# Kernel tuning notes

Hardware: AMD Instinct MI355X
Metric: run time of the kernel (lower is better)

## Reference

```python
import jax, jax.numpy as jnp
import numpy as np

N = 100000          # num nodes
E = 3200000         # num edges (avg degree 32)
G = 64              # num graphs in batch
F_IN = 2            # num_node_features
H = 16              # hidden_size
NUM_LAYERS = 2


def sage_conv(x, src, dst, W_l, b_l, W_r):
    # PyG SAGEConv (mean aggr): out = lin_l(mean_{j in N(i)} x_j) + lin_r(x_i)
    msg = x[src]                                                  # [E, F] gather
    agg = jax.ops.segment_sum(msg, dst, num_segments=N)          # [N, F] scatter-add
    deg = jax.ops.segment_sum(jnp.ones((src.shape[0],), x.dtype), dst, num_segments=N)
    mean = agg / jnp.maximum(deg, 1.0)[:, None]
    return mean @ W_l + b_l + x @ W_r


def setup_inputs() -> dict:
    key = jax.random.key(0)
    ks = jax.random.split(key, 10)
    x = jax.random.normal(ks[0], (N, F_IN), dtype=jnp.float32)
    edge_index = jax.random.randint(ks[1], (2, E), 0, N, dtype=jnp.int64)
    batch = jnp.sort(jax.random.randint(ks[2], (N,), 0, G, dtype=jnp.int64))
    s1 = 1.0 / np.sqrt(F_IN)
    s2 = 1.0 / np.sqrt(H)
    return {
        "x": x,
        "edge_index": edge_index,
        "batch": batch,
        "W1_l": jax.random.uniform(ks[3], (F_IN, H), jnp.float32, -s1, s1),
        "b1_l": jnp.zeros((H,), jnp.float32),
        "W1_r": jax.random.uniform(ks[4], (F_IN, H), jnp.float32, -s1, s1),
        "W2_l": jax.random.uniform(ks[5], (H, H), jnp.float32, -s2, s2),
        "b2_l": jnp.zeros((H,), jnp.float32),
        "W2_r": jax.random.uniform(ks[6], (H, H), jnp.float32, -s2, s2),
        "W_end": jax.random.uniform(ks[7], (H, 1), jnp.float32, -s2, s2),
        "b_end": jnp.zeros((1,), jnp.float32),
    }


def reference(x, edge_index, batch, W1_l, b1_l, W1_r, W2_l, b2_l, W2_r, W_end, b_end):
    src, dst = edge_index[0], edge_index[1]
    h = sage_conv(x, src, dst, W1_l, b1_l, W1_r)                 # conv1
    for _ in range(NUM_LAYERS - 1):
        h = jax.nn.relu(h)
        h = sage_conv(h, src, dst, W2_l, b2_l, W2_r)             # conv2
    h = jax.nn.relu(h)
    # dropout is identity in eval mode
    h = h @ W_end + b_end                                         # [N, 1]
    # global mean pool over graphs
    summed = jax.ops.segment_sum(h, batch, num_segments=G)       # [G, 1]
    counts = jax.ops.segment_sum(jnp.ones((N,), h.dtype), batch, num_segments=G)
    pooled = summed / jnp.maximum(counts, 1.0)[:, None]
    return jax.nn.sigmoid(pooled)                                 # [G, 1]
```

## Files before the change

### kernel.cpp

```cpp
#include <hip/hip_runtime.h>
#include <math.h>

#define NN 100000
#define NE 3200000
#define NG 64
#define HID 16
#define EPB 8192
#define NBLKE ((NE + EPB - 1) / EPB)
#define NBUCK ((NN + 255) / 256)
#define LMAX 10240

typedef unsigned int uint;
typedef float vf2 __attribute__((ext_vector_type(2)));


template <bool HI>
__device__ inline vf2 dec2fp8(uint u) {
#if __has_builtin(__builtin_amdgcn_cvt_pk_f32_fp8)
    return __builtin_amdgcn_cvt_pk_f32_fp8((int)u, HI);
#else
    vf2 r;
    uint b0 = (u >> (HI ? 16 : 0)) & 0xff;
    uint b1 = (u >> (HI ? 24 : 8)) & 0xff;
    uint em0 = b0 & 0x7f, em1 = b1 & 0x7f;
    float v0 = (em0 >= 8) ? __uint_as_float(((em0 >> 3) + 120) << 23 | (em0 & 7) << 20)
                          : (float)em0 * 0.001953125f;
    float v1 = (em1 >= 8) ? __uint_as_float(((em1 >> 3) + 120) << 23 | (em1 & 7) << 20)
                          : (float)em1 * 0.001953125f;
    r.x = (b0 & 0x80) ? -v0 : v0;
    r.y = (b1 & 0x80) ? -v1 : v1;
    return r;
#endif
}

__device__ inline uint enc1fp8(float f) {
    if (!(f > 0.f)) return 0u;
    f = fminf(f, 448.f);
    uint b = __float_as_uint(f);
    int e = (int)(b >> 23) - 127;
    if (e >= -6) {
        uint m = b & 0x7fffffu;
        uint r = (m + 0x7ffffu + ((m >> 20) & 1u)) >> 20;
        uint code = ((uint)(e + 7) << 3) + r;
        return code > 126u ? 126u : code;
    }
    float t = f * 512.f;
    return (uint)(t + 0.5f);
}

template <bool HI>
__device__ inline uint packfp8x2(float a, float b, uint old) {
#if __has_builtin(__builtin_amdgcn_cvt_pk_fp8_f32)
    return (uint)__builtin_amdgcn_cvt_pk_fp8_f32(a, b, (int)old, HI);
#else
    uint v = enc1fp8(a) | (enc1fp8(b) << 8);
    return HI ? ((old & 0x0000ffffu) | (v << 16)) : ((old & 0xffff0000u) | v);
#endif
}

__global__ __launch_bounds__(512) void k_bhist(const int* __restrict__ dst,
                                               int* __restrict__ blockCnt) {
    __shared__ int h[NBUCK];
    int t = threadIdx.x;
    for (int i = t; i < NBUCK; i += 512) h[i] = 0;
    __syncthreads();
    int base = blockIdx.x * EPB;
    int n4 = (min(base + EPB, NE) - base) >> 2;
    const int4* d4 = (const int4*)(dst + base);
    for (int i = t; i < n4; i += 512) {
        int4 v = d4[i];
        atomicAdd(&h[v.x >> 8], 1);
        atomicAdd(&h[v.y >> 8], 1);
        atomicAdd(&h[v.z >> 8], 1);
        atomicAdd(&h[v.w >> 8], 1);
    }
    __syncthreads();
    for (int i = t; i < NBUCK; i += 512)
        blockCnt[i * NBLKE + blockIdx.x] = h[i];
}

__global__ __launch_bounds__(512) void k_bucketscan(int* __restrict__ blockCnt,
                                                    int* __restrict__ bucketTot) {
    __shared__ int a[512];
    int t = threadIdx.x, b = blockIdx.x;
    a[t] = (t < NBLKE) ? blockCnt[b * NBLKE + t] : 0;
    __syncthreads();
    for (int off = 1; off < 512; off <<= 1) {
        int x = a[t] + ((t >= off) ? a[t - off] : 0);
        __syncthreads();
        a[t] = x;
        __syncthreads();
    }
    if (t < NBLKE) blockCnt[b * NBLKE + t] = (t ? a[t - 1] : 0);
    if (t == 0) bucketTot[b] = a[511];
}

__global__ __launch_bounds__(512) void k_basescan(const int* __restrict__ bucketTot,
                                                  int* __restrict__ bucketBase,
                                                  int* __restrict__ offs,
                                                  float* __restrict__ gsum,
                                                  float* __restrict__ gcnt) {
    __shared__ int a[512];
    int t = threadIdx.x;
    if (t < NG) { gsum[t] = 0.f; gcnt[t] = 0.f; }
    a[t] = (t < NBUCK) ? bucketTot[t] : 0;
    __syncthreads();
    for (int off = 1; off < 512; off <<= 1) {
        int x = a[t] + ((t >= off) ? a[t - off] : 0);
        __syncthreads();
        a[t] = x;
        __syncthreads();
    }
    if (t < NBUCK) bucketBase[t] = (t ? a[t - 1] : 0);
    if (t == 0) { bucketBase[NBUCK] = a[511]; offs[NN] = a[511]; }
}

__global__ __launch_bounds__(512) void k_bscatter(const int* __restrict__ src,
                                                  const int* __restrict__ dst,
                                                  const int* __restrict__ blockCnt,
                                                  const int* __restrict__ bucketBase,
                                                  int* __restrict__ pairs) {
    __shared__ int cur[NBUCK];
    int t = threadIdx.x;
    for (int i = t; i < NBUCK; i += 512)
        cur[i] = blockCnt[i * NBLKE + blockIdx.x] + bucketBase[i];
    __syncthreads();
    int base = blockIdx.x * EPB;
    int n4 = (min(base + EPB, NE) - base) >> 2;
    const int4* d4 = (const int4*)(dst + base);
    const int4* s4 = (const int4*)(src + base);
    for (int i = t; i < n4; i += 512) {
        int4 dv = d4[i];
        int4 sv = s4[i];
        int p0 = atomicAdd(&cur[dv.x >> 8], 1);
        pairs[p0] = (sv.x << 8) | (dv.x & 255);
        int p1 = atomicAdd(&cur[dv.y >> 8], 1);
        pairs[p1] = (sv.y << 8) | (dv.y & 255);
        int p2 = atomicAdd(&cur[dv.z >> 8], 1);
        pairs[p2] = (sv.z << 8) | (dv.z & 255);
        int p3 = atomicAdd(&cur[dv.w >> 8], 1);
        pairs[p3] = (sv.w << 8) | (dv.w & 255);
    }
}

__global__ __launch_bounds__(512) void k_fill2c1(
    const int* __restrict__ bucketBase, const int* __restrict__ pairs,
    const float* __restrict__ x,
    const float* __restrict__ W1l, const float* __restrict__ b1l,
    const float* __restrict__ W1r,
    int* __restrict__ offs, int* __restrict__ csr, uint* __restrict__ h8) {
    __shared__ int a[256];
    __shared__ int lcur[256];
    __shared__ int lss[LMAX];
    int t = threadIdx.x, b = blockIdx.x;
    int pb = bucketBase[b], pe = bucketBase[b + 1];
    if (t < 256) a[t] = 0;
    __syncthreads();
    for (int e = pb + t; e < pe; e += 512)
        atomicAdd(&a[pairs[e] & 255], 1);
    __syncthreads();
    for (int off = 1; off < 256; off <<= 1) {
        int v = 0;
        if (t < 256) v = a[t] + ((t >= off) ? a[t - off] : 0);
        __syncthreads();
        if (t < 256) a[t] = v;
        __syncthreads();
    }
    if (t < 256) lcur[t] = t ? a[t - 1] : 0;
    __syncthreads();
    for (int e = pb + t; e < pe; e += 512) {
        int v = pairs[e];
        int s = v >> 8, dl = v & 255;
        int lpos = atomicAdd(&lcur[dl], 1);
        csr[pb + lpos] = s;
        if (lpos < LMAX) lss[lpos] = s;
    }
    __syncthreads();
    if (t < 256) {
        int node = b * 256 + t;
        if (node < NN) {
            int excl = t ? a[t - 1] : 0;
            int cntn = a[t] - excl;
            offs[node] = pb + excl;
            float s0 = 0.f, s1 = 0.f;
            for (int k = 0; k < cntn; ++k) {
                int idx = excl + k;
                int s = (idx < LMAX) ? lss[idx] : csr[pb + idx];
                float2 xv = *(const float2*)(x + 2 * s);
                s0 += xv.x; s1 += xv.y;
            }
            float inv = 1.0f / fmaxf((float)cntn, 1.0f);
            float m0 = s0 * inv, m1 = s1 * inv;
            float x0 = x[2 * node], x1 = x[2 * node + 1];
            float o[16];
#pragma unroll
            for (int h = 0; h < 16; ++h)
                o[h] = fmaxf(m0 * W1l[h] + m1 * W1l[16 + h] + b1l[h]
                           + x0 * W1r[h] + x1 * W1r[16 + h], 0.f);
            uint4 w;
            w.x = packfp8x2<false>(o[0],  o[1],  0u);
            w.x = packfp8x2<true >(o[2],  o[3],  w.x);
            w.y = packfp8x2<false>(o[4],  o[5],  0u);
            w.y = packfp8x2<true >(o[6],  o[7],  w.y);
            w.z = packfp8x2<false>(o[8],  o[9],  0u);
            w.z = packfp8x2<true >(o[10], o[11], w.z);
            w.w = packfp8x2<false>(o[12], o[13], 0u);
            w.w = packfp8x2<true >(o[14], o[15], w.w);
            *(uint4*)(h8 + (size_t)node * 4) = w;
        }
    }
}

__global__ __launch_bounds__(256) void k_conv2pool(
    const int* __restrict__ offs, const int* __restrict__ csr,
    const uint* __restrict__ h8,
    const float* __restrict__ W2l, const float* __restrict__ b2l,
    const float* __restrict__ W2r, const float* __restrict__ Wend,
    const float* __restrict__ bend, const int* __restrict__ batch,
    float* __restrict__ gsum, float* __restrict__ gcnt) {
    __shared__ float sWl[256], sWr[256], sB[HID], sWe[HID];
    __shared__ float sm[64][17], shr[64][17];
    __shared__ float ls[NG], lc[NG];
    int t = threadIdx.x;
    sWl[t] = W2l[t];
    sWr[t] = W2r[t];
    if (t < HID) { sB[t] = b2l[t]; sWe[t] = Wend[t]; }
    if (t < NG) { ls[t] = 0.f; lc[t] = 0.f; }

    int g = t >> 2;
    int l4 = t & 3;
    int gbase = (t & 63) & 60;
    int i = blockIdx.x * 64 + g;
    int beg = 0, end = 0;
    if (i < NN) { beg = offs[i]; end = offs[i + 1]; }
    float a0 = 0.f, a1 = 0.f, a2 = 0.f, a3 = 0.f;
    int kb = beg;
    uint ub[8];
    for (; kb + 8 <= end; kb += 8) {
        int sv0 = csr[kb + l4];
        int sv1 = csr[kb + 4 + l4];
#pragma unroll
        for (int j = 0; j < 4; ++j) {
            int s = __shfl(sv0, gbase + j, 64);
            ub[j] = h8[(size_t)s * 4 + l4];
        }
#pragma unroll
        for (int j = 0; j < 4; ++j) {
            int s = __shfl(sv1, gbase + j, 64);
            ub[4 + j] = h8[(size_t)s * 4 + l4];
        }
#pragma unroll
        for (int j = 0; j < 8; ++j) {
            vf2 p0 = dec2fp8<false>(ub[j]);
            vf2 p1 = dec2fp8<true >(ub[j]);
            a0 += p0.x; a1 += p0.y; a2 += p1.x; a3 += p1.y;
        }
    }
    for (; kb + 4 <= end; kb += 4) {
        int sv = csr[kb + l4];
#pragma unroll
        for (int j = 0; j < 4; ++j) {
            int s = __shfl(sv, gbase + j, 64);
            ub[j] = h8[(size_t)s * 4 + l4];
        }
#pragma unroll
        for (int j = 0; j < 4; ++j) {
            vf2 p0 = dec2fp8<false>(ub[j]);
            vf2 p1 = dec2fp8<true >(ub[j]);
            a0 += p0.x; a1 += p0.y; a2 += p1.x; a3 += p1.y;
        }
    }
    if (kb < end) {
        int idx = kb + l4;
        int sv = (idx < end) ? csr[idx] : 0;
        int nb = end - kb;
        for (int j = 0; j < nb; ++j) {
            int s = __shfl(sv, gbase + j, 64);
            uint u = h8[(size_t)s * 4 + l4];
            vf2 p0 = dec2fp8<false>(u);
            vf2 p1 = dec2fp8<true >(u);
            a0 += p0.x; a1 += p0.y; a2 += p1.x; a3 += p1.y;
        }
    }
    if (i < NN) {
        float inv = 1.0f / fmaxf((float)(end - beg), 1.0f);
        uint us = h8[(size_t)i * 4 + l4];
        vf2 q0 = dec2fp8<false>(us);
        vf2 q1 = dec2fp8<true >(us);
        sm[g][4 * l4 + 0] = a0 * inv;
        sm[g][4 * l4 + 1] = a1 * inv;
        sm[g][4 * l4 + 2] = a2 * inv;
        sm[g][4 * l4 + 3] = a3 * inv;
        shr[g][4 * l4 + 0] = q0.x;
        shr[g][4 * l4 + 1] = q0.y;
        shr[g][4 * l4 + 2] = q1.x;
        shr[g][4 * l4 + 3] = q1.y;
    }
    __syncthreads();

    float y = 0.f;
    if (i < NN) {
#pragma unroll
        for (int k = 0; k < 4; ++k) {
            int h = 4 * l4 + k;
            float a = sB[h];
#pragma unroll
            for (int f = 0; f < HID; ++f)
                a += sm[g][f] * sWl[f * HID + h] + shr[g][f] * sWr[f * HID + h];
            y += fmaxf(a, 0.f) * sWe[h];
        }
    }
    y += __shfl_xor(y, 1, 64);
    y += __shfl_xor(y, 2, 64);
    if (l4 == 0 && i < NN) {
        int bg = batch[i];
        atomicAdd(&ls[bg], y + bend[0]);
        atomicAdd(&lc[bg], 1.0f);
    }
    __syncthreads();
    if (t < NG && lc[t] != 0.0f) {
        unsafeAtomicAdd(&gsum[t], ls[t]);
        unsafeAtomicAdd(&gcnt[t], lc[t]);
    }
}

__global__ void k_final(const float* __restrict__ gsum, const float* __restrict__ gcnt,
                        float* __restrict__ out) {
    int g = threadIdx.x;
    if (g < NG) {
        float p = gsum[g] / fmaxf(gcnt[g], 1.0f);
        out[g] = 1.0f / (1.0f + expf(-p));
    }
}

extern "C" void kernel_launch(void* const* d_in, const int* in_sizes, int n_in,
                              void* d_out, int out_size, void* d_ws, size_t ws_size,
                              hipStream_t stream) {
    const float* x    = (const float*)d_in[0];
    const int*   ei   = (const int*)d_in[1];
    const int*   batch= (const int*)d_in[2];
    const float* W1l  = (const float*)d_in[3];
    const float* b1l  = (const float*)d_in[4];
    const float* W1r  = (const float*)d_in[5];
    const float* W2l  = (const float*)d_in[6];
    const float* b2l  = (const float*)d_in[7];
    const float* W2r  = (const float*)d_in[8];
    const float* Wend = (const float*)d_in[9];
    const float* bend = (const float*)d_in[10];

    const int* src = ei;
    const int* dst = ei + NE;

    float* gsum      = (float*)d_ws;
    float* gcnt      = (float*)d_ws + NG;
    int*   blockCnt  = (int*)d_ws + 2 * NG;
    int*   bucketTot = blockCnt + (size_t)NBLKE * NBUCK;
    int*   bucketBase= bucketTot + NBUCK;
    int*   offs      = bucketBase + NBUCK + 1;
    size_t po        = (size_t)(offs - (int*)d_ws) + NN + 1;
    po               = (po + 3) & ~(size_t)3;
    int*   pairs     = (int*)d_ws + po;
    int*   csr       = pairs + NE;
    uint*  h8        = (uint*)(csr + NE);

    k_bhist     <<<NBLKE, 512, 0, stream>>>(dst, blockCnt);
    k_bucketscan<<<NBUCK, 512, 0, stream>>>(blockCnt, bucketTot);
    k_basescan  <<<1, 512, 0, stream>>>(bucketTot, bucketBase, offs, gsum, gcnt);
    k_bscatter  <<<NBLKE, 512, 0, stream>>>(src, dst, blockCnt, bucketBase, pairs);
    k_fill2c1   <<<NBUCK, 512, 0, stream>>>(bucketBase, pairs, x, W1l, b1l, W1r,
                                            offs, csr, h8);
    k_conv2pool <<<(NN + 63) / 64, 256, 0, stream>>>(offs, csr, h8, W2l, b2l, W2r,
                                                     Wend, bend, batch, gsum, gcnt);
    k_final     <<<1, 64, 0, stream>>>(gsum, gcnt, (float*)d_out);
}
```

Before: 105.5 us.

## Replace global bucket sort with per-block local sort and segmented gather

Merges histogram, scans and scatter into one kernel that sorts each edge chunk locally by destination bucket and writes per-block bucket offsets. The fill kernel then gathers its bucket's segments from every block via a per-bucket scan, writing CSR into fixed-size per-bucket slabs (MAXB) with node offset/count arrays. This cuts four launches and the global prefix-scan passes down to two launches. In exchange, segment reads in fill are serial per thread with short, uncoalesced runs, and the design relies on no bucket exceeding MAXB edges.

```diff
diff --git a/kernel.cpp b/kernel.cpp
--- a/kernel.cpp
+++ b/kernel.cpp
@@ -9,9 +9,11 @@
 #define NBLKE ((NE + EPB - 1) / EPB)
 #define NBUCK ((NN + 255) / 256)
 #define LMAX 10240
+#define MAXB 10240
 
 typedef unsigned int uint;
 typedef float vf2 __attribute__((ext_vector_type(2)));
+typedef int   vi4 __attribute__((ext_vector_type(4)));
 
 
 template <bool HI>
@@ -58,106 +60,106 @@
 #endif
 }
 
-__global__ __launch_bounds__(512) void k_bhist(const int* __restrict__ dst,
-                                               int* __restrict__ blockCnt) {
-    __shared__ int h[NBUCK];
-    int t = threadIdx.x;
-    for (int i = t; i < NBUCK; i += 512) h[i] = 0;
-    __syncthreads();
-    int base = blockIdx.x * EPB;
-    int n4 = (min(base + EPB, NE) - base) >> 2;
-    const int4* d4 = (const int4*)(dst + base);
+__global__ __launch_bounds__(512) void k_sortblk(const int* __restrict__ src,
+                                                 const int* __restrict__ dst,
+                                                 int* __restrict__ blockCnt,
+                                                 int* __restrict__ pairs,
+                                                 float* __restrict__ gsum,
+                                                 float* __restrict__ gcnt) {
+    __shared__ int hist[NBUCK];
+    __shared__ int s[512];
+    __shared__ int cur[NBUCK];
+    int t = threadIdx.x, blk = blockIdx.x;
+    if (blk == 0 && t < NG) { gsum[t] = 0.f; gcnt[t] = 0.f; }
+    for (int i = t; i < NBUCK; i += 512) hist[i] = 0;
+    __syncthreads();
+    int base = blk * EPB;
+    int nE = min(EPB, NE - base);
+    int n4 = nE >> 2;
+    const vi4* d4 = (const vi4*)(dst + base);
+    const vi4* s4 = (const vi4*)(src + base);
     for (int i = t; i < n4; i += 512) {
-        int4 v = d4[i];
-        atomicAdd(&h[v.x >> 8], 1);
-        atomicAdd(&h[v.y >> 8], 1);
-        atomicAdd(&h[v.z >> 8], 1);
-        atomicAdd(&h[v.w >> 8], 1);
-    }
-    __syncthreads();
-    for (int i = t; i < NBUCK; i += 512)
-        blockCnt[i * NBLKE + blockIdx.x] = h[i];
-}
-
-__global__ __launch_bounds__(512) void k_bucketscan(int* __restrict__ blockCnt,
-                                                    int* __restrict__ bucketTot) {
-    __shared__ int a[512];
-    int t = threadIdx.x, b = blockIdx.x;
-    a[t] = (t < NBLKE) ? blockCnt[b * NBLKE + t] : 0;
+        vi4 v = d4[i];
+        atomicAdd(&hist[v.x >> 8], 1);
+        atomicAdd(&hist[v.y >> 8], 1);
+        atomicAdd(&hist[v.z >> 8], 1);
+        atomicAdd(&hist[v.w >> 8], 1);
+    }
+    __syncthreads();
+    s[t] = (t < NBUCK) ? hist[t] : 0;
     __syncthreads();
     for (int off = 1; off < 512; off <<= 1) {
-        int x = a[t] + ((t >= off) ? a[t - off] : 0);
-        __syncthreads();
-        a[t] = x;
-        __syncthreads();
-    }
-    if (t < NBLKE) blockCnt[b * NBLKE + t] = (t ? a[t - 1] : 0);
-    if (t == 0) bucketTot[b] = a[511];
-}
-
-__global__ __launch_bounds__(512) void k_basescan(const int* __restrict__ bucketTot,
-                                                  int* __restrict__ bucketBase,
-                                                  int* __restrict__ offs,
-                                                  float* __restrict__ gsum,
-                                                  float* __restrict__ gcnt) {
-    __shared__ int a[512];
-    int t = threadIdx.x;
-    if (t < NG) { gsum[t] = 0.f; gcnt[t] = 0.f; }
-    a[t] = (t < NBUCK) ? bucketTot[t] : 0;
-    __syncthreads();
-    for (int off = 1; off < 512; off <<= 1) {
-        int x = a[t] + ((t >= off) ? a[t - off] : 0);
-        __syncthreads();
-        a[t] = x;
-        __syncthreads();
-    }
-    if (t < NBUCK) bucketBase[t] = (t ? a[t - 1] : 0);
-    if (t == 0) { bucketBase[NBUCK] = a[511]; offs[NN] = a[511]; }
-}
-
-__global__ __launch_bounds__(512) void k_bscatter(const int* __restrict__ src,
-                                                  const int* __restrict__ dst,
-                                                  const int* __restrict__ blockCnt,
-                                                  const int* __restrict__ bucketBase,
-                                                  int* __restrict__ pairs) {
-    __shared__ int cur[NBUCK];
-    int t = threadIdx.x;
-    for (int i = t; i < NBUCK; i += 512)
-        cur[i] = blockCnt[i * NBLKE + blockIdx.x] + bucketBase[i];
-    __syncthreads();
-    int base = blockIdx.x * EPB;
-    int n4 = (min(base + EPB, NE) - base) >> 2;
-    const int4* d4 = (const int4*)(dst + base);
-    const int4* s4 = (const int4*)(src + base);
+        int x = s[t] + ((t >= off) ? s[t - off] : 0);
+        __syncthreads();
+        s[t] = x;
+        __syncthreads();
+    }
+    int row = blk * (NBUCK + 1);
+    if (t < NBUCK) {
+        int excl = t ? s[t - 1] : 0;
+        blockCnt[row + t] = excl;
+        cur[t] = excl;
+    }
+    if (t == 0) blockCnt[row + NBUCK] = nE;
+    __syncthreads();
     for (int i = t; i < n4; i += 512) {
-        int4 dv = d4[i];
-        int4 sv = s4[i];
+        vi4 dv = d4[i];
+        vi4 sv = s4[i];
         int p0 = atomicAdd(&cur[dv.x >> 8], 1);
-        pairs[p0] = (sv.x << 8) | (dv.x & 255);
+        pairs[base + p0] = (sv.x << 8) | (dv.x & 255);
         int p1 = atomicAdd(&cur[dv.y >> 8], 1);
-        pairs[p1] = (sv.y << 8) | (dv.y & 255);
+        pairs[base + p1] = (sv.y << 8) | (dv.y & 255);
         int p2 = atomicAdd(&cur[dv.z >> 8], 1);
-        pairs[p2] = (sv.z << 8) | (dv.z & 255);
+        pairs[base + p2] = (sv.z << 8) | (dv.z & 255);
         int p3 = atomicAdd(&cur[dv.w >> 8], 1);
-        pairs[p3] = (sv.w << 8) | (dv.w & 255);
+        pairs[base + p3] = (sv.w << 8) | (dv.w & 255);
     }
 }
 
 __global__ __launch_bounds__(512) void k_fill2c1(
-    const int* __restrict__ bucketBase, const int* __restrict__ pairs,
+    const int* __restrict__ blockCnt, const int* __restrict__ pairs,
     const float* __restrict__ x,
     const float* __restrict__ W1l, const float* __restrict__ b1l,
     const float* __restrict__ W1r,
-    int* __restrict__ offs, int* __restrict__ csr, uint* __restrict__ h8) {
+    int* __restrict__ nodeOff, int* __restrict__ nodeCnt,
+    int* __restrict__ csr, uint* __restrict__ h8) {
+    __shared__ int segS[NBLKE];
+    __shared__ int lofs[NBLKE + 1];
+    __shared__ int s[512];
     __shared__ int a[256];
     __shared__ int lcur[256];
-    __shared__ int lss[LMAX];
+    __shared__ int lpair[LMAX];
     int t = threadIdx.x, b = blockIdx.x;
-    int pb = bucketBase[b], pe = bucketBase[b + 1];
+    int segc = 0;
+    if (t < NBLKE) {
+        int row = t * (NBUCK + 1);
+        int o0 = blockCnt[row + b];
+        int o1 = blockCnt[row + b + 1];
+        segS[t] = t * EPB + o0;
+        segc = o1 - o0;
+    }
     if (t < 256) a[t] = 0;
-    __syncthreads();
-    for (int e = pb + t; e < pe; e += 512)
-        atomicAdd(&a[pairs[e] & 255], 1);
+    s[t] = (t < NBLKE) ? segc : 0;
+    __syncthreads();
+    for (int off = 1; off < 512; off <<= 1) {
+        int v = s[t] + ((t >= off) ? s[t - off] : 0);
+        __syncthreads();
+        s[t] = v;
+        __syncthreads();
+    }
+    if (t < NBLKE) lofs[t] = t ? s[t - 1] : 0;
+    if (t == 0) lofs[NBLKE] = s[511];
+    __syncthreads();
+    int tot = lofs[NBLKE];
+    if (t < NBLKE) {
+        int bl = lofs[t];
+        int gs = segS[t];
+        for (int j = 0; j < segc; ++j) {
+            int v = pairs[gs + j];
+            if (bl + j < LMAX) lpair[bl + j] = v;
+            atomicAdd(&a[v & 255], 1);
+        }
+    }
     __syncthreads();
     for (int off = 1; off < 256; off <<= 1) {
         int v = 0;
@@ -168,12 +170,21 @@
     }
     if (t < 256) lcur[t] = t ? a[t - 1] : 0;
     __syncthreads();
-    for (int e = pb + t; e < pe; e += 512) {
-        int v = pairs[e];
-        int s = v >> 8, dl = v & 255;
-        int lpos = atomicAdd(&lcur[dl], 1);
-        csr[pb + lpos] = s;
-        if (lpos < LMAX) lss[lpos] = s;
+    int cbase = b * MAXB;
+    for (int idx = t; idx < tot; idx += 512) {
+        int v;
+        if (idx < LMAX) {
+            v = lpair[idx];
+        } else {
+            int lo = 0, hi = NBLKE - 1;
+            while (lo < hi) {
+                int mid = (lo + hi + 1) >> 1;
+                if (lofs[mid] <= idx) lo = mid; else hi = mid - 1;
+            }
+            v = pairs[segS[lo] + idx - lofs[lo]];
+        }
+        int pos = atomicAdd(&lcur[v & 255], 1);
+        csr[cbase + pos] = v >> 8;
     }
     __syncthreads();
     if (t < 256) {
@@ -181,12 +192,13 @@
         if (node < NN) {
             int excl = t ? a[t - 1] : 0;
             int cntn = a[t] - excl;
-            offs[node] = pb + excl;
+            nodeOff[node] = cbase + excl;
+            nodeCnt[node] = cntn;
             float s0 = 0.f, s1 = 0.f;
+            int gb = cbase + excl;
             for (int k = 0; k < cntn; ++k) {
-                int idx = excl + k;
-                int s = (idx < LMAX) ? lss[idx] : csr[pb + idx];
-                float2 xv = *(const float2*)(x + 2 * s);
+                int sv = csr[gb + k];
+                float2 xv = *(const float2*)(x + 2 * sv);
                 s0 += xv.x; s1 += xv.y;
             }
             float inv = 1.0f / fmaxf((float)cntn, 1.0f);
@@ -212,8 +224,8 @@
 }
 
 __global__ __launch_bounds__(256) void k_conv2pool(
-    const int* __restrict__ offs, const int* __restrict__ csr,
-    const uint* __restrict__ h8,
+    const int* __restrict__ nodeOff, const int* __restrict__ nodeCnt,
+    const int* __restrict__ csr, const uint* __restrict__ h8,
     const float* __restrict__ W2l, const float* __restrict__ b2l,
     const float* __restrict__ W2r, const float* __restrict__ Wend,
     const float* __restrict__ bend, const int* __restrict__ batch,
@@ -232,7 +244,7 @@
     int gbase = (t & 63) & 60;
     int i = blockIdx.x * 64 + g;
     int beg = 0, end = 0;
-    if (i < NN) { beg = offs[i]; end = offs[i + 1]; }
+    if (i < NN) { beg = nodeOff[i]; end = beg + nodeCnt[i]; }
     float a0 = 0.f, a1 = 0.f, a2 = 0.f, a3 = 0.f;
     int kb = beg;
     uint ub[8];
@@ -354,22 +366,19 @@
     float* gsum      = (float*)d_ws;
     float* gcnt      = (float*)d_ws + NG;
     int*   blockCnt  = (int*)d_ws + 2 * NG;
-    int*   bucketTot = blockCnt + (size_t)NBLKE * NBUCK;
-    int*   bucketBase= bucketTot + NBUCK;
-    int*   offs      = bucketBase + NBUCK + 1;
-    size_t po        = (size_t)(offs - (int*)d_ws) + NN + 1;
+    int*   nodeOff   = blockCnt + (size_t)NBLKE * (NBUCK + 1);
+    int*   nodeCnt   = nodeOff + NN;
+    size_t po        = (size_t)(nodeCnt + NN - (int*)d_ws);
     po               = (po + 3) & ~(size_t)3;
     int*   pairs     = (int*)d_ws + po;
     int*   csr       = pairs + NE;
-    uint*  h8        = (uint*)(csr + NE);
-
-    k_bhist     <<<NBLKE, 512, 0, stream>>>(dst, blockCnt);
-    k_bucketscan<<<NBUCK, 512, 0, stream>>>(blockCnt, bucketTot);
-    k_basescan  <<<1, 512, 0, stream>>>(bucketTot, bucketBase, offs, gsum, gcnt);
-    k_bscatter  <<<NBLKE, 512, 0, stream>>>(src, dst, blockCnt, bucketBase, pairs);
-    k_fill2c1   <<<NBUCK, 512, 0, stream>>>(bucketBase, pairs, x, W1l, b1l, W1r,
-                                            offs, csr, h8);
-    k_conv2pool <<<(NN + 63) / 64, 256, 0, stream>>>(offs, csr, h8, W2l, b2l, W2r,
-                                                     Wend, bend, batch, gsum, gcnt);
+    uint*  h8        = (uint*)(csr + (size_t)NBUCK * MAXB);
+
+    k_sortblk   <<<NBLKE, 512, 0, stream>>>(src, dst, blockCnt, pairs, gsum, gcnt);
+    k_fill2c1   <<<NBUCK, 512, 0, stream>>>(blockCnt, pairs, x, W1l, b1l, W1r,
+                                            nodeOff, nodeCnt, csr, h8);
+    k_conv2pool <<<(NN + 63) / 64, 256, 0, stream>>>(nodeOff, nodeCnt, csr, h8,
+                                                     W2l, b2l, W2r, Wend, bend,
+                                                     batch, gsum, gcnt);
     k_final     <<<1, 64, 0, stream>>>(gsum, gcnt, (float*)d_out);
 }
```

Measured after the change: 121.2 us. 1.15x slower.
